# Optimization experiments

Hardware: AMD Instinct MI355X
Metric: run time of the kernel (lower is better)

Reference implementation:

```python
import jax, jax.numpy as jnp
import numpy as np

NUM_HEADS = 32
NUM_KV_HEADS = 8
HEAD_DIM = 128
ROPE_THETA = 10000.0


def _rope_cos_sin(seq_len, head_dim, dtype):
    inv_freq = 1.0 / (ROPE_THETA ** (jnp.arange(0, head_dim, 2, dtype=jnp.float32) / head_dim))
    t = jnp.arange(seq_len, dtype=jnp.float32)
    freqs = jnp.outer(t, inv_freq)              # [S, hd/2]
    emb = jnp.concatenate([freqs, freqs], axis=-1)  # [S, hd]
    return jnp.cos(emb).astype(dtype), jnp.sin(emb).astype(dtype)


def _rotate_half(x):
    h = x.shape[-1] // 2
    return jnp.concatenate([-x[..., h:], x[..., :h]], axis=-1)


def _apply_rope(x, cos, sin):
    # x: [B, H, S, D]; cos/sin: [S, D] (position_ids = arange(S) in prefill)
    return x * cos[None, None] + _rotate_half(x) * sin[None, None]


def setup_inputs() -> dict:
    key = jax.random.key(0)
    ks = jax.random.split(key, 5)
    B, S, H = 1, 2048, 4096
    return {
        "hidden_states": jax.random.normal(ks[0], (B, S, H), dtype=jnp.float32),
        "Wq": jax.random.normal(ks[1], (H, NUM_HEADS * HEAD_DIM), dtype=jnp.float32) * 0.02,
        "Wk": jax.random.normal(ks[2], (H, NUM_KV_HEADS * HEAD_DIM), dtype=jnp.float32) * 0.02,
        "Wv": jax.random.normal(ks[3], (H, NUM_KV_HEADS * HEAD_DIM), dtype=jnp.float32) * 0.02,
        "Wo": jax.random.normal(ks[4], (NUM_HEADS * HEAD_DIM, H), dtype=jnp.float32) * 0.02,
    }


def reference(hidden_states, Wq, Wk, Wv, Wo):
    B, S, H = hidden_states.shape
    nh, nkv, hd = NUM_HEADS, NUM_KV_HEADS, HEAD_DIM
    groups = nh // nkv

    # fused QKV projections (bias-free, Llama-style)
    q = (hidden_states @ Wq).reshape(B, S, nh, hd).transpose(0, 2, 1, 3)   # [B,nh,S,D]
    k = (hidden_states @ Wk).reshape(B, S, nkv, hd).transpose(0, 2, 1, 3)  # [B,nkv,S,D]
    v = (hidden_states @ Wv).reshape(B, S, nkv, hd).transpose(0, 2, 1, 3)

    # inline RoPE on q and k
    cos, sin = _rope_cos_sin(S, hd, q.dtype)
    q = _apply_rope(q, cos, sin)
    k = _apply_rope(k, cos, sin)

    # GQA: repeat kv heads to match query heads (num_key_value_groups)
    k = jnp.repeat(k, groups, axis=1)  # [B,nh,S,D]
    v = jnp.repeat(v, groups, axis=1)

    scale = 1.0 / jnp.sqrt(jnp.asarray(hd, dtype=q.dtype))
    logits = jnp.einsum("bhqd,bhkd->bhqk", q, k) * scale  # [B,nh,S,S]

    # prefill causal mask (phys_past_len = 0)
    causal = jnp.tril(jnp.ones((S, S), dtype=bool))
    neg = jnp.asarray(jnp.finfo(logits.dtype).min, dtype=logits.dtype)
    logits = jnp.where(causal[None, None], logits, neg)

    attn = jax.nn.softmax(logits.astype(jnp.float32), axis=-1).astype(q.dtype)
    out = jnp.einsum("bhqk,bhkd->bhqd", attn, v)           # [B,nh,S,D]
    out = out.transpose(0, 2, 1, 3).reshape(B, S, nh * hd)  # [B,S,H]
    return out @ Wo
```

## Files before the change

kernel.cpp:

```cpp
#include <hip/hip_runtime.h>
#include <cstdint>
#include <cstddef>

typedef __attribute__((ext_vector_type(4))) float f32x4;
typedef __attribute__((ext_vector_type(16))) float f32x16;
typedef __attribute__((ext_vector_type(8))) short bf16x8;
typedef __attribute__((ext_vector_type(2))) unsigned int u32x2;

#define S_LEN   2048
#define HID     4096
#define NH      32
#define NKV     8
#define HD      128
#define QKV_N   6144

typedef const __attribute__((address_space(1))) unsigned int* gptr_t;
typedef __attribute__((address_space(3))) unsigned int* lptr_t;

__device__ __forceinline__ void gload_lds16(const void* g, void* l) {
  __builtin_amdgcn_global_load_lds((gptr_t)g, (lptr_t)l, 16, 0, 0);
}

__device__ __forceinline__ ushort f2bf(float f) {
  union { float f; uint32_t u; } v; v.f = f;
  uint32_t r = v.u + 0x7FFFu + ((v.u >> 16) & 1u);
  return (ushort)(r >> 16);
}
__device__ __forceinline__ float bf2f(ushort u) {
  union { uint32_t u; float f; } v; v.u = ((uint32_t)u) << 16;
  return v.f;
}

__global__ void cast_f32_bf16(const float* __restrict__ in, ushort* __restrict__ out, int n) {
  int i = (blockIdx.x * 256 + threadIdx.x) * 4;
  if (i >= n) return;
  float4 v = *reinterpret_cast<const float4*>(in + i);
  ushort4 o;
  o.x = f2bf(v.x); o.y = f2bf(v.y); o.z = f2bf(v.z); o.w = f2bf(v.w);
  *reinterpret_cast<ushort4*>(out + i) = o;
}

__global__ void transpose_cast(const float* __restrict__ in, ushort* __restrict__ out, int R, int C) {
  __shared__ float t[32][33];
  int tx = threadIdx.x & 31, ty = threadIdx.x >> 5;
  int r0 = blockIdx.y * 32, c0 = blockIdx.x * 32;
#pragma unroll
  for (int i = 0; i < 32; i += 8)
    t[ty + i][tx] = in[(size_t)(r0 + ty + i) * C + c0 + tx];
  __syncthreads();
#pragma unroll
  for (int i = 0; i < 32; i += 8)
    out[(size_t)(c0 + ty + i) * R + r0 + tx] = f2bf(t[tx][ty + i]);
}

template <bool BF16_OUT>
__global__ __launch_bounds__(256, 4) void gemm_bt(
    const ushort* __restrict__ A, const ushort* __restrict__ B,
    void* __restrict__ Cp, int M, int N, int K) {
  __shared__ ushort a_lds[128 * 32];
  __shared__ ushort b_lds[128 * 32];
  const int tid = threadIdx.x;
  const int wid = tid >> 6, lane = tid & 63;
  const int l16 = lane & 15, lk = lane >> 4;
  const int wr = wid >> 1, wc = wid & 1;
  const size_t a_row0 = (size_t)blockIdx.y * 128;
  const size_t b_row0 = (size_t)blockIdx.x * 128;

  f32x4 acc[4][4] = {};
  const int pswz = lk ^ (l16 & 3) ^ ((l16 >> 2) & 1);

  for (int kt = 0; kt < K; kt += 32) {
    __syncthreads();
#pragma unroll
    for (int i = 0; i < 2; ++i) {
      int c = i * 256 + tid;
      int row = c >> 2, p = c & 3;
      int gch = p ^ (row & 3) ^ ((row >> 2) & 1);
      gload_lds16(A + (a_row0 + row) * K + kt + gch * 8, &a_lds[c * 8]);
      gload_lds16(B + (b_row0 + row) * K + kt + gch * 8, &b_lds[c * 8]);
    }
    __syncthreads();

    bf16x8 af[4], bf[4];
#pragma unroll
    for (int m = 0; m < 4; ++m) {
      int row = wr * 64 + m * 16 + l16;
      af[m] = *reinterpret_cast<const bf16x8*>(&a_lds[row * 32 + pswz * 8]);
    }
#pragma unroll
    for (int n = 0; n < 4; ++n) {
      int row = wc * 64 + n * 16 + l16;
      bf[n] = *reinterpret_cast<const bf16x8*>(&b_lds[row * 32 + pswz * 8]);
    }
#pragma unroll
    for (int m = 0; m < 4; ++m)
#pragma unroll
      for (int n = 0; n < 4; ++n)
        acc[m][n] = __builtin_amdgcn_mfma_f32_16x16x32_bf16(af[m], bf[n], acc[m][n], 0, 0, 0);
  }

#pragma unroll
  for (int m = 0; m < 4; ++m) {
    int row_b = wr * 64 + m * 16 + lk * 4;
#pragma unroll
    for (int n = 0; n < 4; ++n) {
      int col = (int)b_row0 + wc * 64 + n * 16 + l16;
#pragma unroll
      for (int r = 0; r < 4; ++r) {
        size_t row = a_row0 + row_b + r;
        if constexpr (BF16_OUT)
          ((ushort*)Cp)[row * N + col] = f2bf(acc[m][n][r]);
        else
          ((float*)Cp)[row * N + col] = acc[m][n][r];
      }
    }
  }
}

__global__ __launch_bounds__(256, 4) void gemm_o_ks(
    const ushort* __restrict__ A, const ushort* __restrict__ B,
    float* __restrict__ P0, float* __restrict__ P1) {
  __shared__ ushort a_lds[128 * 32];
  __shared__ ushort b_lds[128 * 32];
  const int bid = blockIdx.x;
  const int kh = bid >> 9;
  const int rem = bid & 511;
  const size_t b_row0 = (size_t)(rem & 31) * 128;
  const size_t a_row0 = (size_t)(rem >> 5) * 128;
  const int k0 = kh * 2048, k1 = k0 + 2048;
  float* __restrict__ P = kh ? P1 : P0;
  const int tid = threadIdx.x;
  const int wid = tid >> 6, lane = tid & 63;
  const int l16 = lane & 15, lk = lane >> 4;
  const int wr = wid >> 1, wc = wid & 1;

  f32x4 acc[4][4] = {};
  const int pswz = lk ^ (l16 & 3) ^ ((l16 >> 2) & 1);

  for (int kt = k0; kt < k1; kt += 32) {
    __syncthreads();
#pragma unroll
    for (int i = 0; i < 2; ++i) {
      int c = i * 256 + tid;
      int row = c >> 2, p = c & 3;
      int gch = p ^ (row & 3) ^ ((row >> 2) & 1);
      gload_lds16(A + (a_row0 + row) * HID + kt + gch * 8, &a_lds[c * 8]);
      gload_lds16(B + (b_row0 + row) * HID + kt + gch * 8, &b_lds[c * 8]);
    }
    __syncthreads();

    bf16x8 af[4], bf[4];
#pragma unroll
    for (int m = 0; m < 4; ++m) {
      int row = wr * 64 + m * 16 + l16;
      af[m] = *reinterpret_cast<const bf16x8*>(&a_lds[row * 32 + pswz * 8]);
    }
#pragma unroll
    for (int n = 0; n < 4; ++n) {
      int row = wc * 64 + n * 16 + l16;
      bf[n] = *reinterpret_cast<const bf16x8*>(&b_lds[row * 32 + pswz * 8]);
    }
#pragma unroll
    for (int m = 0; m < 4; ++m)
#pragma unroll
      for (int n = 0; n < 4; ++n)
        acc[m][n] = __builtin_amdgcn_mfma_f32_16x16x32_bf16(af[m], bf[n], acc[m][n], 0, 0, 0);
  }

#pragma unroll
  for (int m = 0; m < 4; ++m) {
    int row_b = wr * 64 + m * 16 + lk * 4;
#pragma unroll
    for (int n = 0; n < 4; ++n) {
      int col = (int)b_row0 + wc * 64 + n * 16 + l16;
#pragma unroll
      for (int r = 0; r < 4; ++r)
        P[(a_row0 + row_b + r) * HID + col] = acc[m][n][r];
    }
  }
}

__global__ void add_f32(const float* __restrict__ a, const float* __restrict__ b,
                        float* __restrict__ o, int n) {
  int i = (blockIdx.x * 256 + threadIdx.x) * 4;
  if (i >= n) return;
  float4 x = *reinterpret_cast<const float4*>(a + i);
  float4 y = *reinterpret_cast<const float4*>(b + i);
  float4 z; z.x = x.x + y.x; z.y = x.y + y.y; z.z = x.z + y.z; z.w = x.w + y.w;
  *reinterpret_cast<float4*>(o + i) = z;
}

__global__ void rope_kernel(ushort* __restrict__ QKV) {
  int idx = blockIdx.x * 256 + threadIdx.x;
  int dg = idx & 7;
  int t = idx >> 3;
  int s = t / 40;
  int hh = t - s * 40;
  if (s >= S_LEN) return;
  int col = (hh < NH) ? hh * HD : HID + (hh - NH) * HD;
  ushort* base = QKV + (size_t)s * QKV_N + col + dg * 8;

  union U { uint4 v; ushort u[8]; };
  U L, H, OL, OH;
  L.v = *reinterpret_cast<const uint4*>(base);
  H.v = *reinterpret_cast<const uint4*>(base + 64);
  const float C0 = 13.287712379549449f / 64.0f;
#pragma unroll
  for (int j = 0; j < 8; ++j) {
    int d = dg * 8 + j;
    float invf = exp2f(-(float)d * C0);
    float ang = (float)s * invf;
    float sn, cs;
    sincosf(ang, &sn, &cs);
    float xl = bf2f(L.u[j]), xh = bf2f(H.u[j]);
    OL.u[j] = f2bf(xl * cs - xh * sn);
    OH.u[j] = f2bf(xh * cs + xl * sn);
  }
  *reinterpret_cast<uint4*>(base) = OL.v;
  *reinterpret_cast<uint4*>(base + 64) = OH.v;
}

__global__ void transpose_v(const ushort* __restrict__ QKV, ushort* __restrict__ Vt) {
  __shared__ ushort t[64][65];
  int s0 = blockIdx.x * 64;
  int d0 = blockIdx.y * 64;
  int hkv = blockIdx.z;
  int tx = threadIdx.x & 63, ty = threadIdx.x >> 6;
#pragma unroll
  for (int i = 0; i < 64; i += 4)
    t[i + ty][tx] = QKV[(size_t)(s0 + i + ty) * QKV_N + HID + NKV * HD + hkv * HD + d0 + tx];
  __syncthreads();
#pragma unroll
  for (int i = 0; i < 64; i += 4)
    Vt[((size_t)hkv * HD + d0 + i + ty) * S_LEN + s0 + tx] = t[tx][i + ty];
}

__global__ __launch_bounds__(512, 2) void attn_kernel(
    const ushort* __restrict__ QKV, const ushort* __restrict__ Vt, ushort* __restrict__ AO) {
  constexpr float SCALE = 0.08838834764831845f;
  __shared__ ushort k_lds[2][64 * 128];
  __shared__ ushort v_lds[2][128 * 64];

  const int lin = blockIdx.x;
  const int h = ((lin & 7) << 2) + ((lin >> 3) & 3);
  const int pr = lin >> 5;
  const int hkv = h >> 2;
  const int tid = threadIdx.x, w = tid >> 6, lane = tid & 63;
  const int l32 = lane & 31;
  const int hi = lane >> 5;
  const int qb = (w < 4) ? (15 - pr) : pr;
  const int q0w = qb * 128 + (w & 3) * 32;
  const int qg = q0w + l32;

  bf16x8 qf[8];
  {
    const ushort* qrow = QKV + (size_t)qg * QKV_N + h * HD + hi * 8;
#pragma unroll
    for (int ds = 0; ds < 8; ++ds)
      qf[ds] = *reinterpret_cast<const bf16x8*>(qrow + ds * 16);
  }

  float m_run = -1e30f, l_run = 0.f;
  f32x16 oacc[4] = {};

  auto stageKV = [&](int buf, int kt) {
#pragma unroll
    for (int i = 0; i < 2; ++i) {
      int c = i * 512 + tid;
      int row = c >> 4, ch = c & 15;
      int sch = ch ^ (row & 7);
      gload_lds16(QKV + (size_t)(kt * 64 + row) * QKV_N + HID + hkv * HD + sch * 8,
                  &k_lds[buf][c * 8]);
    }
#pragma unroll
    for (int i = 0; i < 2; ++i) {
      int c = i * 512 + tid;
      int row = c >> 3, ch = c & 7;
      int sch = ch ^ (row & 7);
      gload_lds16(Vt + ((size_t)hkv * HD + row) * S_LEN + (size_t)kt * 64 + sch * 8,
                  &v_lds[buf][c * 8]);
    }
  };

  const int NT = 34 - 2 * pr;
  stageKV(0, 0);
  __syncthreads();

  for (int kt = 0; kt < NT; ++kt) {
    const int cur = kt & 1;
    if (kt + 1 < NT) stageKV(cur ^ 1, kt + 1);

    if (kt * 64 <= q0w + 31) {
      float pv[32];
      __builtin_amdgcn_s_setprio(1);
#pragma unroll
      for (int kf = 0; kf < 2; ++kf) {
        f32x16 s = {};
        int rk = kf * 32 + l32;
#pragma unroll
        for (int ds = 0; ds < 8; ++ds) {
          int c16 = (ds * 2 + hi) ^ (rk & 7);
          bf16x8 kfr = *reinterpret_cast<const bf16x8*>(&k_lds[cur][rk * 128 + c16 * 8]);
          s = __builtin_amdgcn_mfma_f32_32x32x16_bf16(kfr, qf[ds], s, 0, 0, 0);
        }
#pragma unroll
        for (int r = 0; r < 16; ++r) pv[kf * 16 + r] = s[r] * SCALE;
      }
      __builtin_amdgcn_s_setprio(0);

      if (kt * 64 + 63 > q0w) {
#pragma unroll
        for (int kf = 0; kf < 2; ++kf)
#pragma unroll
          for (int r = 0; r < 16; ++r) {
            int kl = kf * 32 + (r & 3) + 8 * (r >> 2) + 4 * hi;
            if (kt * 64 + kl > qg) pv[kf * 16 + r] = -1e30f;
          }
      }

      float mt = pv[0];
#pragma unroll
      for (int i = 1; i < 32; ++i) mt = fmaxf(mt, pv[i]);
      mt = fmaxf(mt, __shfl_xor(mt, 32, 64));
      float mn = fmaxf(m_run, mt);
      float alpha = __expf(m_run - mn);
      float ls = 0.f;
#pragma unroll
      for (int i = 0; i < 32; ++i) { pv[i] = __expf(pv[i] - mn); ls += pv[i]; }
      ls += __shfl_xor(ls, 32, 64);
      l_run = l_run * alpha + ls;
      m_run = mn;
#pragma unroll
      for (int f = 0; f < 4; ++f)
#pragma unroll
        for (int r = 0; r < 16; ++r) oacc[f][r] *= alpha;

      union PW { uint32_t w[4]; bf16x8 v; } pa[4];
#pragma unroll
      for (int ks = 0; ks < 4; ++ks) {
        uint32_t x0, x1, y0, y1;
        asm("v_cvt_pk_bf16_f32 %0, %1, %2" : "=v"(x0) : "v"(pv[8 * ks + 0]), "v"(pv[8 * ks + 1]));
        asm("v_cvt_pk_bf16_f32 %0, %1, %2" : "=v"(x1) : "v"(pv[8 * ks + 2]), "v"(pv[8 * ks + 3]));
        asm("v_cvt_pk_bf16_f32 %0, %1, %2" : "=v"(y0) : "v"(pv[8 * ks + 4]), "v"(pv[8 * ks + 5]));
        asm("v_cvt_pk_bf16_f32 %0, %1, %2" : "=v"(y1) : "v"(pv[8 * ks + 6]), "v"(pv[8 * ks + 7]));
        u32x2 r0 = __builtin_amdgcn_permlane32_swap(x0, y0, false, false);
        u32x2 r1 = __builtin_amdgcn_permlane32_swap(x1, y1, false, false);
        pa[ks].w[0] = r0.x; pa[ks].w[1] = r1.x; pa[ks].w[2] = r0.y; pa[ks].w[3] = r1.y;
      }

      __builtin_amdgcn_s_setprio(1);
#pragma unroll
      for (int ks = 0; ks < 4; ++ks) {
#pragma unroll
        for (int f = 0; f < 4; ++f) {
          int dv = f * 32 + l32;
          int c8 = (2 * ks + hi) ^ (dv & 7);
          bf16x8 vfr = *reinterpret_cast<const bf16x8*>(&v_lds[cur][dv * 64 + c8 * 8]);
          oacc[f] = __builtin_amdgcn_mfma_f32_32x32x16_bf16(vfr, pa[ks].v, oacc[f], 0, 0, 0);
        }
      }
      __builtin_amdgcn_s_setprio(0);
    }

    __syncthreads();
  }

  float inv_l = 1.0f / l_run;
  ushort* aorow = AO + (size_t)qg * HID + h * HD;
#pragma unroll
  for (int f = 0; f < 4; ++f)
#pragma unroll
    for (int g = 0; g < 4; ++g) {
      ushort4 o;
      o.x = f2bf(oacc[f][g * 4 + 0] * inv_l);
      o.y = f2bf(oacc[f][g * 4 + 1] * inv_l);
      o.z = f2bf(oacc[f][g * 4 + 2] * inv_l);
      o.w = f2bf(oacc[f][g * 4 + 3] * inv_l);
      *reinterpret_cast<ushort4*>(aorow + f * 32 + g * 8 + 4 * hi) = o;
    }
}

extern "C" void kernel_launch(void* const* d_in, const int* in_sizes, int n_in,
                              void* d_out, int out_size, void* d_ws, size_t ws_size,
                              hipStream_t stream) {
  (void)in_sizes; (void)n_in; (void)out_size;
  const float* hs = (const float*)d_in[0];
  const float* Wq = (const float*)d_in[1];
  const float* Wk = (const float*)d_in[2];
  const float* Wv = (const float*)d_in[3];
  const float* Wo = (const float*)d_in[4];
  float* out = (float*)d_out;

  char* ws = (char*)d_ws;
  const size_t OFF_HSB   = 0;
  const size_t OFF_WQKVT = OFF_HSB + 16777216;
  const size_t OFF_WOT   = OFF_WQKVT + 50331648;
  const size_t OFF_QKV   = OFF_WOT + 33554432;
  const size_t OFF_VT    = OFF_QKV + 25165824;
  const size_t OFF_AO    = OFF_VT + 4194304;
  if (ws_size < OFF_AO + 16777216) return;

  ushort* hsb   = (ushort*)(ws + OFF_HSB);
  ushort* WqkvT = (ushort*)(ws + OFF_WQKVT);
  ushort* WoT   = (ushort*)(ws + OFF_WOT);
  ushort* QKV   = (ushort*)(ws + OFF_QKV);
  ushort* Vt    = (ushort*)(ws + OFF_VT);
  ushort* AO    = (ushort*)(ws + OFF_AO);
  float* P0 = (float*)(ws + 0);
  float* P1 = (float*)(ws + 33554432);

  cast_f32_bf16<<<8192, 256, 0, stream>>>(hs, hsb, S_LEN * HID);
  transpose_cast<<<dim3(4096 / 32, 4096 / 32), 256, 0, stream>>>(Wq, WqkvT, HID, 4096);
  transpose_cast<<<dim3(1024 / 32, 4096 / 32), 256, 0, stream>>>(Wk, WqkvT + (size_t)4096 * HID, HID, 1024);
  transpose_cast<<<dim3(1024 / 32, 4096 / 32), 256, 0, stream>>>(Wv, WqkvT + (size_t)5120 * HID, HID, 1024);
  transpose_cast<<<dim3(4096 / 32, 4096 / 32), 256, 0, stream>>>(Wo, WoT, 4096, HID);

  gemm_bt<true><<<dim3(QKV_N / 128, S_LEN / 128), 256, 0, stream>>>(hsb, WqkvT, QKV, S_LEN, QKV_N, HID);
  rope_kernel<<<(S_LEN * 40 * 8) / 256, 256, 0, stream>>>(QKV);
  transpose_v<<<dim3(S_LEN / 64, HD / 64, NKV), 256, 0, stream>>>(QKV, Vt);
  attn_kernel<<<256, 512, 0, stream>>>(QKV, Vt, AO);
  gemm_o_ks<<<1024, 256, 0, stream>>>(AO, WoT, P0, P1);
  add_f32<<<8192, 256, 0, stream>>>(P0, P1, out, S_LEN * HID);
}
```

Before: 362.0 us.

## Merge prep kernels and restructure attention to process paired q-blocks sequentially

The four weight transpose-cast launches become one launch, and RoPE plus the V transpose become one launch, to cut launch overhead. The attention kernel drops from 512 to 256 threads per block. Each block now runs its two paired q-blocks (p and 15-p) one after the other with 4 waves each, instead of 8 waves working on both at once. This reduces shared K/V staging reuse and halves the waves per block, so attention could lose latency hiding and take longer.

```diff
diff --git a/kernel.cpp b/kernel.cpp
--- a/kernel.cpp
+++ b/kernel.cpp
@@ -40,17 +40,27 @@
   *reinterpret_cast<ushort4*>(out + i) = o;
 }
 
-__global__ void transpose_cast(const float* __restrict__ in, ushort* __restrict__ out, int R, int C) {
+__global__ void transpose_cast_all(const float* __restrict__ Wq, const float* __restrict__ Wk,
+                                   const float* __restrict__ Wv, const float* __restrict__ Wo,
+                                   ushort* __restrict__ WqkvT, ushort* __restrict__ WoT) {
   __shared__ float t[32][33];
+  int id = blockIdx.x;
+  const float* src; ushort* dst; int C, local;
+  if (id < 16384)        { src = Wq; dst = WqkvT;                           C = 4096; local = id; }
+  else if (id < 20480)   { src = Wk; dst = WqkvT + (size_t)4096 * HID;      C = 1024; local = id - 16384; }
+  else if (id < 24576)   { src = Wv; dst = WqkvT + (size_t)5120 * HID;      C = 1024; local = id - 20480; }
+  else                   { src = Wo; dst = WoT;                             C = 4096; local = id - 24576; }
+  const int cb = C >> 5;
+  int bx = local % cb, by = local / cb;
   int tx = threadIdx.x & 31, ty = threadIdx.x >> 5;
-  int r0 = blockIdx.y * 32, c0 = blockIdx.x * 32;
+  int r0 = by * 32, c0 = bx * 32;
 #pragma unroll
   for (int i = 0; i < 32; i += 8)
-    t[ty + i][tx] = in[(size_t)(r0 + ty + i) * C + c0 + tx];
+    t[ty + i][tx] = src[(size_t)(r0 + ty + i) * C + c0 + tx];
   __syncthreads();
 #pragma unroll
   for (int i = 0; i < 32; i += 8)
-    out[(size_t)(c0 + ty + i) * R + r0 + tx] = f2bf(t[tx][ty + i]);
+    dst[(size_t)(c0 + ty + i) * 4096 + r0 + tx] = f2bf(t[tx][ty + i]);
 }
 
 template <bool BF16_OUT>
@@ -190,52 +200,53 @@
   *reinterpret_cast<float4*>(o + i) = z;
 }
 
-__global__ void rope_kernel(ushort* __restrict__ QKV) {
-  int idx = blockIdx.x * 256 + threadIdx.x;
-  int dg = idx & 7;
-  int t = idx >> 3;
-  int s = t / 40;
-  int hh = t - s * 40;
-  if (s >= S_LEN) return;
-  int col = (hh < NH) ? hh * HD : HID + (hh - NH) * HD;
-  ushort* base = QKV + (size_t)s * QKV_N + col + dg * 8;
-
-  union U { uint4 v; ushort u[8]; };
-  U L, H, OL, OH;
-  L.v = *reinterpret_cast<const uint4*>(base);
-  H.v = *reinterpret_cast<const uint4*>(base + 64);
-  const float C0 = 13.287712379549449f / 64.0f;
-#pragma unroll
-  for (int j = 0; j < 8; ++j) {
-    int d = dg * 8 + j;
-    float invf = exp2f(-(float)d * C0);
-    float ang = (float)s * invf;
-    float sn, cs;
-    sincosf(ang, &sn, &cs);
-    float xl = bf2f(L.u[j]), xh = bf2f(H.u[j]);
-    OL.u[j] = f2bf(xl * cs - xh * sn);
-    OH.u[j] = f2bf(xh * cs + xl * sn);
-  }
-  *reinterpret_cast<uint4*>(base) = OL.v;
-  *reinterpret_cast<uint4*>(base + 64) = OH.v;
-}
-
-__global__ void transpose_v(const ushort* __restrict__ QKV, ushort* __restrict__ Vt) {
-  __shared__ ushort t[64][65];
-  int s0 = blockIdx.x * 64;
-  int d0 = blockIdx.y * 64;
-  int hkv = blockIdx.z;
-  int tx = threadIdx.x & 63, ty = threadIdx.x >> 6;
-#pragma unroll
-  for (int i = 0; i < 64; i += 4)
-    t[i + ty][tx] = QKV[(size_t)(s0 + i + ty) * QKV_N + HID + NKV * HD + hkv * HD + d0 + tx];
-  __syncthreads();
-#pragma unroll
-  for (int i = 0; i < 64; i += 4)
-    Vt[((size_t)hkv * HD + d0 + i + ty) * S_LEN + s0 + tx] = t[tx][i + ty];
-}
-
-__global__ __launch_bounds__(512, 2) void attn_kernel(
+__global__ void rope_and_tv(ushort* __restrict__ QKV, ushort* __restrict__ Vt) {
+  if (blockIdx.x < 2560) {
+    int idx = blockIdx.x * 256 + threadIdx.x;
+    int dg = idx & 7;
+    int t = idx >> 3;
+    int s = t / 40;
+    int hh = t - s * 40;
+    if (s >= S_LEN) return;
+    int col = (hh < NH) ? hh * HD : HID + (hh - NH) * HD;
+    ushort* base = QKV + (size_t)s * QKV_N + col + dg * 8;
+
+    union U { uint4 v; ushort u[8]; };
+    U L, H, OL, OH;
+    L.v = *reinterpret_cast<const uint4*>(base);
+    H.v = *reinterpret_cast<const uint4*>(base + 64);
+    const float C0 = 13.287712379549449f / 64.0f;
+#pragma unroll
+    for (int j = 0; j < 8; ++j) {
+      int d = dg * 8 + j;
+      float invf = exp2f(-(float)d * C0);
+      float ang = (float)s * invf;
+      float sn, cs;
+      sincosf(ang, &sn, &cs);
+      float xl = bf2f(L.u[j]), xh = bf2f(H.u[j]);
+      OL.u[j] = f2bf(xl * cs - xh * sn);
+      OH.u[j] = f2bf(xh * cs + xl * sn);
+    }
+    *reinterpret_cast<uint4*>(base) = OL.v;
+    *reinterpret_cast<uint4*>(base + 64) = OH.v;
+  } else {
+    __shared__ ushort t[64][65];
+    int local = blockIdx.x - 2560;
+    int s0 = (local & 31) * 64;
+    int d0 = ((local >> 5) & 1) * 64;
+    int hkv = local >> 6;
+    int tx = threadIdx.x & 63, ty = threadIdx.x >> 6;
+#pragma unroll
+    for (int i = 0; i < 64; i += 4)
+      t[i + ty][tx] = QKV[(size_t)(s0 + i + ty) * QKV_N + HID + NKV * HD + hkv * HD + d0 + tx];
+    __syncthreads();
+#pragma unroll
+    for (int i = 0; i < 64; i += 4)
+      Vt[((size_t)hkv * HD + d0 + i + ty) * S_LEN + s0 + tx] = t[tx][i + ty];
+  }
+}
+
+__global__ __launch_bounds__(256, 2) void attn_kernel(
     const ushort* __restrict__ QKV, const ushort* __restrict__ Vt, ushort* __restrict__ AO) {
   constexpr float SCALE = 0.08838834764831845f;
   __shared__ ushort k_lds[2][64 * 128];
@@ -243,38 +254,24 @@
 
   const int lin = blockIdx.x;
   const int h = ((lin & 7) << 2) + ((lin >> 3) & 3);
-  const int pr = lin >> 5;
+  const int p = lin >> 5;
   const int hkv = h >> 2;
-  const int tid = threadIdx.x, w = tid >> 6, lane = tid & 63;
+  const int tid = threadIdx.x, wid = tid >> 6, lane = tid & 63;
   const int l32 = lane & 31;
   const int hi = lane >> 5;
-  const int qb = (w < 4) ? (15 - pr) : pr;
-  const int q0w = qb * 128 + (w & 3) * 32;
-  const int qg = q0w + l32;
-
-  bf16x8 qf[8];
-  {
-    const ushort* qrow = QKV + (size_t)qg * QKV_N + h * HD + hi * 8;
-#pragma unroll
-    for (int ds = 0; ds < 8; ++ds)
-      qf[ds] = *reinterpret_cast<const bf16x8*>(qrow + ds * 16);
-  }
-
-  float m_run = -1e30f, l_run = 0.f;
-  f32x16 oacc[4] = {};
 
   auto stageKV = [&](int buf, int kt) {
 #pragma unroll
-    for (int i = 0; i < 2; ++i) {
-      int c = i * 512 + tid;
+    for (int i = 0; i < 4; ++i) {
+      int c = i * 256 + wid * 64 + lane;
       int row = c >> 4, ch = c & 15;
       int sch = ch ^ (row & 7);
       gload_lds16(QKV + (size_t)(kt * 64 + row) * QKV_N + HID + hkv * HD + sch * 8,
                   &k_lds[buf][c * 8]);
     }
 #pragma unroll
-    for (int i = 0; i < 2; ++i) {
-      int c = i * 512 + tid;
+    for (int i = 0; i < 4; ++i) {
+      int c = i * 256 + wid * 64 + lane;
       int row = c >> 3, ch = c & 7;
       int sch = ch ^ (row & 7);
       gload_lds16(Vt + ((size_t)hkv * HD + row) * S_LEN + (size_t)kt * 64 + sch * 8,
@@ -282,102 +279,119 @@
     }
   };
 
-  const int NT = 34 - 2 * pr;
-  stageKV(0, 0);
-  __syncthreads();
-
-  for (int kt = 0; kt < NT; ++kt) {
-    const int cur = kt & 1;
-    if (kt + 1 < NT) stageKV(cur ^ 1, kt + 1);
-
-    if (kt * 64 <= q0w + 31) {
-      float pv[32];
-      __builtin_amdgcn_s_setprio(1);
-#pragma unroll
-      for (int kf = 0; kf < 2; ++kf) {
-        f32x16 s = {};
-        int rk = kf * 32 + l32;
-#pragma unroll
-        for (int ds = 0; ds < 8; ++ds) {
-          int c16 = (ds * 2 + hi) ^ (rk & 7);
-          bf16x8 kfr = *reinterpret_cast<const bf16x8*>(&k_lds[cur][rk * 128 + c16 * 8]);
-          s = __builtin_amdgcn_mfma_f32_32x32x16_bf16(kfr, qf[ds], s, 0, 0, 0);
+  for (int pi = 0; pi < 2; ++pi) {
+    const int qb = pi ? (15 - p) : p;
+    const int q0 = qb * 128;
+    const int qg = q0 + wid * 32 + l32;
+
+    bf16x8 qf[8];
+    {
+      const ushort* qrow = QKV + (size_t)qg * QKV_N + h * HD + hi * 8;
+#pragma unroll
+      for (int ds = 0; ds < 8; ++ds)
+        qf[ds] = *reinterpret_cast<const bf16x8*>(qrow + ds * 16);
+    }
+
+    float m_run = -1e30f, l_run = 0.f;
+    f32x16 oacc[4] = {};
+
+    stageKV(0, 0);
+    __syncthreads();
+
+    const int nt = 2 * qb + 2;
+    for (int kt = 0; kt < nt; ++kt) {
+      const int cur = kt & 1;
+      if (kt + 1 < nt) stageKV(cur ^ 1, kt + 1);
+
+      if (kt * 64 <= q0 + wid * 32 + 31) {
+        float pv[32];
+        __builtin_amdgcn_s_setprio(1);
+#pragma unroll
+        for (int kf = 0; kf < 2; ++kf) {
+          f32x16 s = {};
+          int rk = kf * 32 + l32;
+#pragma unroll
+          for (int ds = 0; ds < 8; ++ds) {
+            int c16 = (ds * 2 + hi) ^ (rk & 7);
+            bf16x8 kfr = *reinterpret_cast<const bf16x8*>(&k_lds[cur][rk * 128 + c16 * 8]);
+            s = __builtin_amdgcn_mfma_f32_32x32x16_bf16(kfr, qf[ds], s, 0, 0, 0);
+          }
+#pragma unroll
+          for (int r = 0; r < 16; ++r) pv[kf * 16 + r] = s[r] * SCALE;
         }
-#pragma unroll
-        for (int r = 0; r < 16; ++r) pv[kf * 16 + r] = s[r] * SCALE;
+        __builtin_amdgcn_s_setprio(0);
+
+        if (kt * 64 + 63 > q0 + wid * 32) {
+#pragma unroll
+          for (int kf = 0; kf < 2; ++kf)
+#pragma unroll
+            for (int r = 0; r < 16; ++r) {
+              int kl = kf * 32 + (r & 3) + 8 * (r >> 2) + 4 * hi;
+              if (kt * 64 + kl > qg) pv[kf * 16 + r] = -1e30f;
+            }
+        }
+
+        float mt = pv[0];
+#pragma unroll
+        for (int i = 1; i < 32; ++i) mt = fmaxf(mt, pv[i]);
+        mt = fmaxf(mt, __shfl_xor(mt, 32, 64));
+        float mn = fmaxf(m_run, mt);
+        float alpha = __expf(m_run - mn);
+        float ls = 0.f;
+#pragma unroll
+        for (int i = 0; i < 32; ++i) { pv[i] = __expf(pv[i] - mn); ls += pv[i]; }
+        ls += __shfl_xor(ls, 32, 64);
+        l_run = l_run * alpha + ls;
+        m_run = mn;
+#pragma unroll
+        for (int f = 0; f < 4; ++f)
+#pragma unroll
+          for (int r = 0; r < 16; ++r) oacc[f][r] *= alpha;
+
+        union PW { uint32_t w[4]; bf16x8 v; } pa[4];
+#pragma unroll
+        for (int ks = 0; ks < 4; ++ks) {
+          uint32_t x0, x1, y0, y1;
+          asm("v_cvt_pk_bf16_f32 %0, %1, %2" : "=v"(x0) : "v"(pv[8 * ks + 0]), "v"(pv[8 * ks + 1]));
+          asm("v_cvt_pk_bf16_f32 %0, %1, %2" : "=v"(x1) : "v"(pv[8 * ks + 2]), "v"(pv[8 * ks + 3]));
+          asm("v_cvt_pk_bf16_f32 %0, %1, %2" : "=v"(y0) : "v"(pv[8 * ks + 4]), "v"(pv[8 * ks + 5]));
+          asm("v_cvt_pk_bf16_f32 %0, %1, %2" : "=v"(y1) : "v"(pv[8 * ks + 6]), "v"(pv[8 * ks + 7]));
+          u32x2 r0 = __builtin_amdgcn_permlane32_swap(x0, y0, false, false);
+          u32x2 r1 = __builtin_amdgcn_permlane32_swap(x1, y1, false, false);
+          pa[ks].w[0] = r0.x; pa[ks].w[1] = r1.x; pa[ks].w[2] = r0.y; pa[ks].w[3] = r1.y;
+        }
+
+        __builtin_amdgcn_s_setprio(1);
+#pragma unroll
+        for (int ks = 0; ks < 4; ++ks) {
+#pragma unroll
+          for (int f = 0; f < 4; ++f) {
+            int dv = f * 32 + l32;
+            int c8 = (2 * ks + hi) ^ (dv & 7);
+            bf16x8 vfr = *reinterpret_cast<const bf16x8*>(&v_lds[cur][dv * 64 + c8 * 8]);
+            oacc[f] = __builtin_amdgcn_mfma_f32_32x32x16_bf16(vfr, pa[ks].v, oacc[f], 0, 0, 0);
+          }
+        }
+        __builtin_amdgcn_s_setprio(0);
       }
-      __builtin_amdgcn_s_setprio(0);
-
-      if (kt * 64 + 63 > q0w) {
-#pragma unroll
-        for (int kf = 0; kf < 2; ++kf)
-#pragma unroll
-          for (int r = 0; r < 16; ++r) {
-            int kl = kf * 32 + (r & 3) + 8 * (r >> 2) + 4 * hi;
-            if (kt * 64 + kl > qg) pv[kf * 16 + r] = -1e30f;
-          }
+
+      __syncthreads();
+    }
+
+    float inv_l = 1.0f / l_run;
+    ushort* aorow = AO + (size_t)qg * HID + h * HD;
+#pragma unroll
+    for (int f = 0; f < 4; ++f)
+#pragma unroll
+      for (int g = 0; g < 4; ++g) {
+        ushort4 o;
+        o.x = f2bf(oacc[f][g * 4 + 0] * inv_l);
+        o.y = f2bf(oacc[f][g * 4 + 1] * inv_l);
+        o.z = f2bf(oacc[f][g * 4 + 2] * inv_l);
+        o.w = f2bf(oacc[f][g * 4 + 3] * inv_l);
+        *reinterpret_cast<ushort4*>(aorow + f * 32 + g * 8 + 4 * hi) = o;
       }
-
-      float mt = pv[0];
-#pragma unroll
-      for (int i = 1; i < 32; ++i) mt = fmaxf(mt, pv[i]);
-      mt = fmaxf(mt, __shfl_xor(mt, 32, 64));
-      float mn = fmaxf(m_run, mt);
-      float alpha = __expf(m_run - mn);
-      float ls = 0.f;
-#pragma unroll
-      for (int i = 0; i < 32; ++i) { pv[i] = __expf(pv[i] - mn); ls += pv[i]; }
-      ls += __shfl_xor(ls, 32, 64);
-      l_run = l_run * alpha + ls;
-      m_run = mn;
-#pragma unroll
-      for (int f = 0; f < 4; ++f)
-#pragma unroll
-        for (int r = 0; r < 16; ++r) oacc[f][r] *= alpha;
-
-      union PW { uint32_t w[4]; bf16x8 v; } pa[4];
-#pragma unroll
-      for (int ks = 0; ks < 4; ++ks) {
-        uint32_t x0, x1, y0, y1;
-        asm("v_cvt_pk_bf16_f32 %0, %1, %2" : "=v"(x0) : "v"(pv[8 * ks + 0]), "v"(pv[8 * ks + 1]));
-        asm("v_cvt_pk_bf16_f32 %0, %1, %2" : "=v"(x1) : "v"(pv[8 * ks + 2]), "v"(pv[8 * ks + 3]));
-        asm("v_cvt_pk_bf16_f32 %0, %1, %2" : "=v"(y0) : "v"(pv[8 * ks + 4]), "v"(pv[8 * ks + 5]));
-        asm("v_cvt_pk_bf16_f32 %0, %1, %2" : "=v"(y1) : "v"(pv[8 * ks + 6]), "v"(pv[8 * ks + 7]));
-        u32x2 r0 = __builtin_amdgcn_permlane32_swap(x0, y0, false, false);
-        u32x2 r1 = __builtin_amdgcn_permlane32_swap(x1, y1, false, false);
-        pa[ks].w[0] = r0.x; pa[ks].w[1] = r1.x; pa[ks].w[2] = r0.y; pa[ks].w[3] = r1.y;
-      }
-
-      __builtin_amdgcn_s_setprio(1);
-#pragma unroll
-      for (int ks = 0; ks < 4; ++ks) {
-#pragma unroll
-        for (int f = 0; f < 4; ++f) {
-          int dv = f * 32 + l32;
-          int c8 = (2 * ks + hi) ^ (dv & 7);
-          bf16x8 vfr = *reinterpret_cast<const bf16x8*>(&v_lds[cur][dv * 64 + c8 * 8]);
-          oacc[f] = __builtin_amdgcn_mfma_f32_32x32x16_bf16(vfr, pa[ks].v, oacc[f], 0, 0, 0);
-        }
-      }
-      __builtin_amdgcn_s_setprio(0);
-    }
-
-    __syncthreads();
-  }
-
-  float inv_l = 1.0f / l_run;
-  ushort* aorow = AO + (size_t)qg * HID + h * HD;
-#pragma unroll
-  for (int f = 0; f < 4; ++f)
-#pragma unroll
-    for (int g = 0; g < 4; ++g) {
-      ushort4 o;
-      o.x = f2bf(oacc[f][g * 4 + 0] * inv_l);
-      o.y = f2bf(oacc[f][g * 4 + 1] * inv_l);
-      o.z = f2bf(oacc[f][g * 4 + 2] * inv_l);
-      o.w = f2bf(oacc[f][g * 4 + 3] * inv_l);
-      *reinterpret_cast<ushort4*>(aorow + f * 32 + g * 8 + 4 * hi) = o;
-    }
+  }
 }
 
 extern "C" void kernel_launch(void* const* d_in, const int* in_sizes, int n_in,
@@ -410,15 +424,11 @@
   float* P1 = (float*)(ws + 33554432);
 
   cast_f32_bf16<<<8192, 256, 0, stream>>>(hs, hsb, S_LEN * HID);
-  transpose_cast<<<dim3(4096 / 32, 4096 / 32), 256, 0, stream>>>(Wq, WqkvT, HID, 4096);
-  transpose_cast<<<dim3(1024 / 32, 4096 / 32), 256, 0, stream>>>(Wk, WqkvT + (size_t)4096 * HID, HID, 1024);
-  transpose_cast<<<dim3(1024 / 32, 4096 / 32), 256, 0, stream>>>(Wv, WqkvT + (size_t)5120 * HID, HID, 1024);
-  transpose_cast<<<dim3(4096 / 32, 4096 / 32), 256, 0, stream>>>(Wo, WoT, 4096, HID);
+  transpose_cast_all<<<40960, 256, 0, stream>>>(Wq, Wk, Wv, Wo, WqkvT, WoT);
 
   gemm_bt<true><<<dim3(QKV_N / 128, S_LEN / 128), 256, 0, stream>>>(hsb, WqkvT, QKV, S_LEN, QKV_N, HID);
-  rope_kernel<<<(S_LEN * 40 * 8) / 256, 256, 0, stream>>>(QKV);
-  transpose_v<<<dim3(S_LEN / 64, HD / 64, NKV), 256, 0, stream>>>(QKV, Vt);
-  attn_kernel<<<256, 512, 0, stream>>>(QKV, Vt, AO);
+  rope_and_tv<<<3072, 256, 0, stream>>>(QKV, Vt);
+  attn_kernel<<<256, 256, 0, stream>>>(QKV, Vt, AO);
   gemm_o_ks<<<1024, 256, 0, stream>>>(AO, WoT, P0, P1);
   add_f32<<<8192, 256, 0, stream>>>(P0, P1, out, S_LEN * HID);
 }
```

Result: faster. 352.0 us (-2.8%).
